# Kernel optimization log

Hardware: AMD Instinct MI355X
Metric: run time of the kernel (lower is better)

## Reference

```python
import jax, jax.numpy as jnp
import numpy as np

BOOST_STRENGTH = 1.0  # from init kwargs, already >= 0


def setup_inputs() -> dict:
    key = jax.random.key(0)
    k1, k2 = jax.random.split(key)
    B, C, H, W = 64, 128, 56, 56
    x = jax.random.normal(k1, (B, C, H, W), dtype=jnp.float32)
    # duty cycles are running activation frequencies in [0, 1]
    duty_cycles = jax.random.uniform(k2, (1, C, 1, 1), dtype=jnp.float32)
    k = 40141  # round(0.1 * C*H*W)
    return {"x": x, "duty_cycles": duty_cycles, "k": k}


def reference(x, duty_cycles, k):
    B = x.shape[0]
    n = x.shape[1] * x.shape[2] * x.shape[3]
    target_density = jnp.float32(k / n)
    # boosting only selects winners; original (unboosted) values are kept
    boost_factors = jnp.exp((target_density - duty_cycles) * BOOST_STRENGTH)
    boosted = (x * boost_factors).reshape(B, -1)   # [B, n]
    flat_x = x.reshape(B, -1)                      # [B, n]
    _, idx = jax.lax.top_k(boosted, k)             # [B, k]
    winners = jnp.take_along_axis(flat_x, idx, axis=1)  # original values at winning units
    res = jnp.zeros_like(flat_x).at[jnp.arange(B)[:, None], idx].set(winners)
    return res.reshape(x.shape)
```

## Files before the change

### kernel.cpp

```cpp
#include <hip/hip_runtime.h>
#include <stdint.h>

#define BB 64
#define CC 128
#define HW 3136
#define NPR (CC * HW)
#define NBINS 8192
#define BIN_SHIFT 19
#define KEY_LOW 0x7FFFFu

typedef float vf4 __attribute__((ext_vector_type(4)));

#define ROWMETA_OFF 512
#define COUNTER_OFF 2048
#define HIST_OFF 4096
#define CAND_OFF (HIST_OFF + (size_t)BB * NBINS * 4)

__device__ __forceinline__ uint32_t tokey(float b) {
    uint32_t u = __float_as_uint(b);
    return u ^ (uint32_t)(((int32_t)u >> 31) | 0x80000000);
}

__device__ __forceinline__ float boostf(const float* dc, int c, int K) {
    float td = (float)((double)K / (double)NPR);
    float d = td - dc[c];
    return (float)exp((double)d);
}

__global__ __launch_bounds__(256) void k_hist(const float* __restrict__ x,
                                              const float* __restrict__ dc,
                                              const int* __restrict__ kptr,
                                              uint32_t* __restrict__ hist) {
    __shared__ uint32_t lh[NBINS];
    __shared__ float sbf[8];
    for (int i = threadIdx.x; i < NBINS; i += 256) lh[i] = 0;
    if (threadIdx.x < 8) {
        int c0 = (blockIdx.x & 15) * 8;
        sbf[threadIdx.x] = boostf(dc, c0 + threadIdx.x, *kptr);
    }
    __syncthreads();

    int row = blockIdx.x >> 4;
    int c0 = (blockIdx.x & 15) * 8;
    const float4* xp = (const float4*)(x + (size_t)row * NPR + (size_t)c0 * HW);
    const int nf4 = 8 * HW / 4;

    int t = threadIdx.x;
    for (; t + 256 < nf4; t += 512) {
        float4 a = xp[t];
        float4 b = xp[t + 256];
        float fa = sbf[t / 784];
        float fb = sbf[(t + 256) / 784];
        atomicAdd(&lh[tokey(a.x * fa) >> BIN_SHIFT], 1u);
        atomicAdd(&lh[tokey(a.y * fa) >> BIN_SHIFT], 1u);
        atomicAdd(&lh[tokey(a.z * fa) >> BIN_SHIFT], 1u);
        atomicAdd(&lh[tokey(a.w * fa) >> BIN_SHIFT], 1u);
        atomicAdd(&lh[tokey(b.x * fb) >> BIN_SHIFT], 1u);
        atomicAdd(&lh[tokey(b.y * fb) >> BIN_SHIFT], 1u);
        atomicAdd(&lh[tokey(b.z * fb) >> BIN_SHIFT], 1u);
        atomicAdd(&lh[tokey(b.w * fb) >> BIN_SHIFT], 1u);
    }
    if (t < nf4) {
        float4 a = xp[t];
        float fa = sbf[t / 784];
        atomicAdd(&lh[tokey(a.x * fa) >> BIN_SHIFT], 1u);
        atomicAdd(&lh[tokey(a.y * fa) >> BIN_SHIFT], 1u);
        atomicAdd(&lh[tokey(a.z * fa) >> BIN_SHIFT], 1u);
        atomicAdd(&lh[tokey(a.w * fa) >> BIN_SHIFT], 1u);
    }
    __syncthreads();
    uint32_t* gh = hist + (size_t)row * NBINS;
    for (int i = threadIdx.x; i < NBINS; i += 256) {
        uint32_t v = lh[i];
        if (v) atomicAdd(&gh[i], v);
    }
}

__global__ __launch_bounds__(256) void k_scan(const uint32_t* __restrict__ hist,
                                              const int* __restrict__ kptr,
                                              int2* __restrict__ rowmeta) {
    int row = blockIdx.x;
    const uint32_t* gh = hist + (size_t)row * NBINS;
    uint32_t K = (uint32_t)(*kptr);
    __shared__ uint32_t csum[256];
    int t = threadIdx.x;
    int hi = NBINS - 1 - 32 * t;
    uint32_t s = 0;
    for (int j = 0; j < 32; j++) s += gh[hi - j];
    csum[t] = s;
    __syncthreads();
    for (int off = 1; off < 256; off <<= 1) {
        uint32_t v = (t >= off) ? csum[t - off] : 0u;
        __syncthreads();
        csum[t] += v;
        __syncthreads();
    }
    uint32_t incl = csum[t];
    uint32_t excl = incl - s;
    if (excl < K && incl >= K) {
        uint32_t cum = excl;
        for (int j = 0; j < 32; j++) {
            int b = hi - j;
            uint32_t h = gh[b];
            if (cum + h >= K) { rowmeta[row] = make_int2(b, (int)(K - cum)); break; }
            cum += h;
        }
    }
}

__global__ __launch_bounds__(256) void k_write(const float* __restrict__ x,
                                               const float* __restrict__ dc,
                                               const int* __restrict__ kptr,
                                               const int2* __restrict__ rowmeta,
                                               float* __restrict__ out,
                                               unsigned long long* __restrict__ cand,
                                               uint32_t* __restrict__ counters,
                                               int cap) {
    int row = blockIdx.x >> 4;
    int c0 = (blockIdx.x & 15) * 8;
    int bstar = rowmeta[row].x;

    __shared__ float sbf[8];
    __shared__ uint32_t lcnt;
    __shared__ uint32_t gbase;
    __shared__ unsigned long long lbuf[2048];
    if (threadIdx.x == 0) lcnt = 0;
    if (threadIdx.x < 8) sbf[threadIdx.x] = boostf(dc, c0 + threadIdx.x, *kptr);
    __syncthreads();

    size_t base = (size_t)row * NPR + (size_t)c0 * HW;
    const float4* xp = (const float4*)(x + base);
    vf4* op = (vf4*)(out + base);
    int jbase = c0 * HW;
    const int nf4 = 8 * HW / 4;

    int t = threadIdx.x;
    for (; t + 256 < nf4; t += 512) {
        float4 a = xp[t];
        float4 b = xp[t + 256];
        float fa = sbf[t / 784];
        float fb = sbf[(t + 256) / 784];
        vf4 oa, ob;
        float* ai = (float*)&a;
        float* bi = (float*)&b;
        #pragma unroll
        for (int q = 0; q < 4; q++) {
            float xv = ai[q];
            uint32_t key = tokey(xv * fa);
            int bin = (int)(key >> BIN_SHIFT);
            oa[q] = (bin > bstar) ? xv : 0.0f;
            if (bin == bstar) {
                uint32_t j = (uint32_t)(jbase + 4 * t + q);
                unsigned long long packed =
                    ((unsigned long long)(key & KEY_LOW) << 32) | (uint32_t)(~j);
                uint32_t pos = atomicAdd(&lcnt, 1u);
                if (pos < 2048u) lbuf[pos] = packed;
                else {
                    uint32_t gp = atomicAdd(&counters[row], 1u);
                    if ((int)gp < cap) cand[(size_t)row * cap + gp] = packed;
                }
            }
        }
        #pragma unroll
        for (int q = 0; q < 4; q++) {
            float xv = bi[q];
            uint32_t key = tokey(xv * fb);
            int bin = (int)(key >> BIN_SHIFT);
            ob[q] = (bin > bstar) ? xv : 0.0f;
            if (bin == bstar) {
                uint32_t j = (uint32_t)(jbase + 4 * (t + 256) + q);
                unsigned long long packed =
                    ((unsigned long long)(key & KEY_LOW) << 32) | (uint32_t)(~j);
                uint32_t pos = atomicAdd(&lcnt, 1u);
                if (pos < 2048u) lbuf[pos] = packed;
                else {
                    uint32_t gp = atomicAdd(&counters[row], 1u);
                    if ((int)gp < cap) cand[(size_t)row * cap + gp] = packed;
                }
            }
        }
        __builtin_nontemporal_store(oa, &op[t]);
        __builtin_nontemporal_store(ob, &op[t + 256]);
    }
    if (t < nf4) {
        float4 a = xp[t];
        float fa = sbf[t / 784];
        vf4 oa;
        float* ai = (float*)&a;
        #pragma unroll
        for (int q = 0; q < 4; q++) {
            float xv = ai[q];
            uint32_t key = tokey(xv * fa);
            int bin = (int)(key >> BIN_SHIFT);
            oa[q] = (bin > bstar) ? xv : 0.0f;
            if (bin == bstar) {
                uint32_t j = (uint32_t)(jbase + 4 * t + q);
                unsigned long long packed =
                    ((unsigned long long)(key & KEY_LOW) << 32) | (uint32_t)(~j);
                uint32_t pos = atomicAdd(&lcnt, 1u);
                if (pos < 2048u) lbuf[pos] = packed;
                else {
                    uint32_t gp = atomicAdd(&counters[row], 1u);
                    if ((int)gp < cap) cand[(size_t)row * cap + gp] = packed;
                }
            }
        }
        __builtin_nontemporal_store(oa, &op[t]);
    }
    __syncthreads();
    uint32_t m = lcnt < 2048u ? lcnt : 2048u;
    if (threadIdx.x == 0) gbase = atomicAdd(&counters[row], m);
    __syncthreads();
    for (uint32_t i = threadIdx.x; i < m; i += 256) {
        uint32_t pos = gbase + i;
        if ((int)pos < cap) cand[(size_t)row * cap + pos] = lbuf[i];
    }
}

__global__ __launch_bounds__(1024) void k_select(const float* __restrict__ x,
                                                 float* __restrict__ out,
                                                 const unsigned long long* __restrict__ cand,
                                                 const uint32_t* __restrict__ counters,
                                                 const int2* __restrict__ rowmeta,
                                                 int cap) {
    int row = blockIdx.x;
    uint32_t cnt = counters[row];
    if ((int)cnt > cap) cnt = (uint32_t)cap;
    int E = rowmeta[row].y;
    const unsigned long long* cp = cand + (size_t)row * cap;
    int tid = threadIdx.x;

    __shared__ uint32_t hist[256];
    __shared__ uint32_t sufs[256];
    __shared__ unsigned long long buf[6144];
    __shared__ uint32_t scnt;
    __shared__ int sh_d, sh_done;

    unsigned long long prefix = 0ull, mask = 0ull, thr = 0ull;
    uint32_t remaining = (uint32_t)E;
    bool compacted = false;
    uint32_t csize = cnt;
    if (tid == 0) sh_done = 0;

    for (int shift = 48; shift >= 0; shift -= 8) {
        if (tid < 256) hist[tid] = 0;
        __syncthreads();
        if (!compacted) {
            for (uint32_t s = tid; s < cnt; s += 1024) {
                unsigned long long v = cp[s];
                if ((v & mask) == prefix)
                    atomicAdd(&hist[(uint32_t)(v >> shift) & 255u], 1u);
            }
        } else {
            for (uint32_t s = tid; s < csize; s += 1024)
                atomicAdd(&hist[(uint32_t)(buf[s] >> shift) & 255u], 1u);
        }
        __syncthreads();
        if (tid < 256) sufs[tid] = hist[tid];
        __syncthreads();
        for (int off = 1; off < 256; off <<= 1) {
            uint32_t add = 0;
            if (tid < 256 && tid + off < 256) add = sufs[tid + off];
            __syncthreads();
            if (tid < 256) sufs[tid] += add;
            __syncthreads();
        }
        if (tid < 256) {
            uint32_t sd = sufs[tid];
            uint32_t sn = (tid < 255) ? sufs[tid + 1] : 0u;
            if (sd >= remaining && sn < remaining) sh_d = tid;
        }
        __syncthreads();
        int d = sh_d;
        uint32_t cumG = (d < 255) ? sufs[d + 1] : 0u;
        uint32_t binC = sufs[d] - cumG;
        unsigned long long npref = prefix | ((unsigned long long)(uint32_t)d << shift);
        bool done = (sufs[d] == remaining);
        if (done) {
            thr = npref;
            if (tid == 0) sh_done = 1;
        }
        remaining -= cumG;
        __syncthreads();
        if (!sh_done && binC <= 6144u && shift > 0) {
            if (tid == 0) scnt = 0;
            unsigned long long keep[6]; int nk = 0;
            if (compacted) {
                for (uint32_t s = tid; s < csize; s += 1024) {
                    unsigned long long v = buf[s];
                    if (((uint32_t)(v >> shift) & 255u) == (uint32_t)d) {
                        if (nk < 6) keep[nk++] = v;
                    }
                }
            }
            __syncthreads();
            if (!compacted) {
                for (uint32_t s = tid; s < cnt; s += 1024) {
                    unsigned long long v = cp[s];
                    if ((v & mask) == prefix &&
                        ((uint32_t)(v >> shift) & 255u) == (uint32_t)d) {
                        uint32_t p = atomicAdd(&scnt, 1u);
                        buf[p] = v;
                    }
                }
            } else if (nk > 0) {
                uint32_t p = atomicAdd(&scnt, (uint32_t)nk);
                for (int i = 0; i < nk; i++) buf[p + i] = keep[i];
            }
            __syncthreads();
            csize = binC;
            compacted = true;
        }
        prefix = npref;
        mask |= (0xFFull << shift);
        if (sh_done) break;
    }
    if (!sh_done) thr = prefix;

    const float* xr = x + (size_t)row * NPR;
    float* orow = out + (size_t)row * NPR;
    for (uint32_t s = tid; s < cnt; s += 1024) {
        unsigned long long v = cp[s];
        if (v >= thr) {
            uint32_t j = ~(uint32_t)v;
            orow[j] = xr[j];
        }
    }
}

extern "C" void kernel_launch(void* const* d_in, const int* in_sizes, int n_in,
                              void* d_out, int out_size, void* d_ws, size_t ws_size,
                              hipStream_t stream) {
    const float* x  = (const float*)d_in[0];
    const float* dc = (const float*)d_in[1];
    const int* kptr = (const int*)d_in[2];
    float* out = (float*)d_out;

    char* ws = (char*)d_ws;
    int2* rowmeta       = (int2*)(ws + ROWMETA_OFF);
    uint32_t* counters  = (uint32_t*)(ws + COUNTER_OFF);
    uint32_t* hist      = (uint32_t*)(ws + HIST_OFF);
    unsigned long long* cand = (unsigned long long*)(ws + CAND_OFF);

    size_t cap_sz = (ws_size > CAND_OFF) ? (ws_size - CAND_OFF) / ((size_t)BB * 8) : 0;
    if (cap_sz > 65536) cap_sz = 65536;
    int cap = (int)cap_sz;

    (void)hipMemsetAsync(ws, 0, CAND_OFF, stream);
    k_hist<<<BB * 16, 256, 0, stream>>>(x, dc, kptr, hist);
    k_scan<<<BB, 256, 0, stream>>>(hist, kptr, rowmeta);
    k_write<<<BB * 16, 256, 0, stream>>>(x, dc, kptr, rowmeta, out, cand, counters, cap);
    k_select<<<BB, 1024, 0, stream>>>(x, out, cand, counters, rowmeta, cap);
}
```

Measured before the change: 224.2 us.

## Fuse row scan and select into last-arriving block via done counters

Removes the separate k_scan and k_select launches. The last of the 16 blocks per row now does the threshold scan at the end of k_hist and the radix select at the end of k_write, detected through atomic done counters. Select runs with 256 threads and reuses the 2048-entry lbuf shared buffer instead of a 6144-entry buffer, so the compaction threshold is lower. This saves launch gaps and tail latency, but the per-row select runs on fewer threads and is serialized behind the slowest block of each row.

```diff
diff --git a/kernel.cpp b/kernel.cpp
--- a/kernel.cpp
+++ b/kernel.cpp
@@ -13,6 +13,8 @@
 
 #define ROWMETA_OFF 512
 #define COUNTER_OFF 2048
+#define DONE1_OFF 2560
+#define DONE2_OFF 2816
 #define HIST_OFF 4096
 #define CAND_OFF (HIST_OFF + (size_t)BB * NBINS * 4)
 
@@ -27,12 +29,23 @@
     return (float)exp((double)d);
 }
 
+__device__ __forceinline__ uint32_t aload32(const uint32_t* p) {
+    return __hip_atomic_load(p, __ATOMIC_RELAXED, __HIP_MEMORY_SCOPE_AGENT);
+}
+__device__ __forceinline__ unsigned long long aload64(const unsigned long long* p) {
+    return __hip_atomic_load(p, __ATOMIC_RELAXED, __HIP_MEMORY_SCOPE_AGENT);
+}
+
 __global__ __launch_bounds__(256) void k_hist(const float* __restrict__ x,
                                               const float* __restrict__ dc,
                                               const int* __restrict__ kptr,
-                                              uint32_t* __restrict__ hist) {
+                                              uint32_t* __restrict__ hist,
+                                              uint32_t* __restrict__ done1,
+                                              int2* __restrict__ rowmeta) {
     __shared__ uint32_t lh[NBINS];
     __shared__ float sbf[8];
+    __shared__ uint32_t csum[256];
+    __shared__ int sh_last;
     for (int i = threadIdx.x; i < NBINS; i += 256) lh[i] = 0;
     if (threadIdx.x < 8) {
         int c0 = (blockIdx.x & 15) * 8;
@@ -74,34 +87,35 @@
         uint32_t v = lh[i];
         if (v) atomicAdd(&gh[i], v);
     }
-}
-
-__global__ __launch_bounds__(256) void k_scan(const uint32_t* __restrict__ hist,
-                                              const int* __restrict__ kptr,
-                                              int2* __restrict__ rowmeta) {
-    int row = blockIdx.x;
-    const uint32_t* gh = hist + (size_t)row * NBINS;
+
+    if (threadIdx.x == 0) {
+        uint32_t prev = __hip_atomic_fetch_add(&done1[row], 1u,
+                          __ATOMIC_ACQ_REL, __HIP_MEMORY_SCOPE_AGENT);
+        sh_last = (prev == 15);
+    }
+    __syncthreads();
+    if (!sh_last) return;
+
     uint32_t K = (uint32_t)(*kptr);
-    __shared__ uint32_t csum[256];
-    int t = threadIdx.x;
-    int hi = NBINS - 1 - 32 * t;
+    int tt = threadIdx.x;
+    int hi = NBINS - 1 - 32 * tt;
     uint32_t s = 0;
-    for (int j = 0; j < 32; j++) s += gh[hi - j];
-    csum[t] = s;
+    for (int j = 0; j < 32; j++) s += aload32(&gh[hi - j]);
+    csum[tt] = s;
     __syncthreads();
     for (int off = 1; off < 256; off <<= 1) {
-        uint32_t v = (t >= off) ? csum[t - off] : 0u;
-        __syncthreads();
-        csum[t] += v;
-        __syncthreads();
-    }
-    uint32_t incl = csum[t];
+        uint32_t v = (tt >= off) ? csum[tt - off] : 0u;
+        __syncthreads();
+        csum[tt] += v;
+        __syncthreads();
+    }
+    uint32_t incl = csum[tt];
     uint32_t excl = incl - s;
     if (excl < K && incl >= K) {
         uint32_t cum = excl;
         for (int j = 0; j < 32; j++) {
             int b = hi - j;
-            uint32_t h = gh[b];
+            uint32_t h = aload32(&gh[b]);
             if (cum + h >= K) { rowmeta[row] = make_int2(b, (int)(K - cum)); break; }
             cum += h;
         }
@@ -115,15 +129,17 @@
                                                float* __restrict__ out,
                                                unsigned long long* __restrict__ cand,
                                                uint32_t* __restrict__ counters,
+                                               uint32_t* __restrict__ done2,
                                                int cap) {
     int row = blockIdx.x >> 4;
     int c0 = (blockIdx.x & 15) * 8;
-    int bstar = rowmeta[row].x;
+    int2 rm = rowmeta[row];
+    int bstar = rm.x;
 
     __shared__ float sbf[8];
-    __shared__ uint32_t lcnt;
-    __shared__ uint32_t gbase;
+    __shared__ uint32_t lcnt, gbase;
     __shared__ unsigned long long lbuf[2048];
+    __shared__ int sh_last;
     if (threadIdx.x == 0) lcnt = 0;
     if (threadIdx.x < 8) sbf[threadIdx.x] = boostf(dc, c0 + threadIdx.x, *kptr);
     __syncthreads();
@@ -215,57 +231,54 @@
         uint32_t pos = gbase + i;
         if ((int)pos < cap) cand[(size_t)row * cap + pos] = lbuf[i];
     }
-}
-
-__global__ __launch_bounds__(1024) void k_select(const float* __restrict__ x,
-                                                 float* __restrict__ out,
-                                                 const unsigned long long* __restrict__ cand,
-                                                 const uint32_t* __restrict__ counters,
-                                                 const int2* __restrict__ rowmeta,
-                                                 int cap) {
-    int row = blockIdx.x;
-    uint32_t cnt = counters[row];
+
+    if (threadIdx.x == 0) {
+        uint32_t prev = __hip_atomic_fetch_add(&done2[row], 1u,
+                          __ATOMIC_ACQ_REL, __HIP_MEMORY_SCOPE_AGENT);
+        sh_last = (prev == 15);
+    }
+    __syncthreads();
+    if (!sh_last) return;
+
+    uint32_t cnt = aload32(&counters[row]);
     if ((int)cnt > cap) cnt = (uint32_t)cap;
-    int E = rowmeta[row].y;
+    uint32_t remaining = (uint32_t)rm.y;
     const unsigned long long* cp = cand + (size_t)row * cap;
     int tid = threadIdx.x;
 
-    __shared__ uint32_t hist[256];
+    __shared__ uint32_t hh[256];
     __shared__ uint32_t sufs[256];
-    __shared__ unsigned long long buf[6144];
     __shared__ uint32_t scnt;
     __shared__ int sh_d, sh_done;
 
     unsigned long long prefix = 0ull, mask = 0ull, thr = 0ull;
-    uint32_t remaining = (uint32_t)E;
     bool compacted = false;
     uint32_t csize = cnt;
     if (tid == 0) sh_done = 0;
 
     for (int shift = 48; shift >= 0; shift -= 8) {
-        if (tid < 256) hist[tid] = 0;
+        hh[tid] = 0;
         __syncthreads();
         if (!compacted) {
-            for (uint32_t s = tid; s < cnt; s += 1024) {
-                unsigned long long v = cp[s];
+            for (uint32_t s = tid; s < cnt; s += 256) {
+                unsigned long long v = aload64(&cp[s]);
                 if ((v & mask) == prefix)
-                    atomicAdd(&hist[(uint32_t)(v >> shift) & 255u], 1u);
+                    atomicAdd(&hh[(uint32_t)(v >> shift) & 255u], 1u);
             }
         } else {
-            for (uint32_t s = tid; s < csize; s += 1024)
-                atomicAdd(&hist[(uint32_t)(buf[s] >> shift) & 255u], 1u);
-        }
-        __syncthreads();
-        if (tid < 256) sufs[tid] = hist[tid];
+            for (uint32_t s = tid; s < csize; s += 256)
+                atomicAdd(&hh[(uint32_t)(lbuf[s] >> shift) & 255u], 1u);
+        }
+        __syncthreads();
+        sufs[tid] = hh[tid];
         __syncthreads();
         for (int off = 1; off < 256; off <<= 1) {
-            uint32_t add = 0;
-            if (tid < 256 && tid + off < 256) add = sufs[tid + off];
+            uint32_t add = (tid + off < 256) ? sufs[tid + off] : 0u;
             __syncthreads();
-            if (tid < 256) sufs[tid] += add;
+            sufs[tid] += add;
             __syncthreads();
         }
-        if (tid < 256) {
+        {
             uint32_t sd = sufs[tid];
             uint32_t sn = (tid < 255) ? sufs[tid + 1] : 0u;
             if (sd >= remaining && sn < remaining) sh_d = tid;
@@ -275,37 +288,36 @@
         uint32_t cumG = (d < 255) ? sufs[d + 1] : 0u;
         uint32_t binC = sufs[d] - cumG;
         unsigned long long npref = prefix | ((unsigned long long)(uint32_t)d << shift);
-        bool done = (sufs[d] == remaining);
-        if (done) {
+        bool done_ = (sufs[d] == remaining);
+        if (done_) {
             thr = npref;
             if (tid == 0) sh_done = 1;
         }
         remaining -= cumG;
         __syncthreads();
-        if (!sh_done && binC <= 6144u && shift > 0) {
+        if (!sh_done && binC <= 2048u && shift > 0) {
             if (tid == 0) scnt = 0;
-            unsigned long long keep[6]; int nk = 0;
+            unsigned long long keep[8]; int nk = 0;
             if (compacted) {
-                for (uint32_t s = tid; s < csize; s += 1024) {
-                    unsigned long long v = buf[s];
-                    if (((uint32_t)(v >> shift) & 255u) == (uint32_t)d) {
-                        if (nk < 6) keep[nk++] = v;
-                    }
+                for (uint32_t s = tid; s < csize; s += 256) {
+                    unsigned long long v = lbuf[s];
+                    if (((uint32_t)(v >> shift) & 255u) == (uint32_t)d && nk < 8)
+                        keep[nk++] = v;
                 }
             }
             __syncthreads();
             if (!compacted) {
-                for (uint32_t s = tid; s < cnt; s += 1024) {
-                    unsigned long long v = cp[s];
+                for (uint32_t s = tid; s < cnt; s += 256) {
+                    unsigned long long v = aload64(&cp[s]);
                     if ((v & mask) == prefix &&
                         ((uint32_t)(v >> shift) & 255u) == (uint32_t)d) {
                         uint32_t p = atomicAdd(&scnt, 1u);
-                        buf[p] = v;
+                        lbuf[p] = v;
                     }
                 }
             } else if (nk > 0) {
                 uint32_t p = atomicAdd(&scnt, (uint32_t)nk);
-                for (int i = 0; i < nk; i++) buf[p + i] = keep[i];
+                for (int i = 0; i < nk; i++) lbuf[p + i] = keep[i];
             }
             __syncthreads();
             csize = binC;
@@ -319,8 +331,8 @@
 
     const float* xr = x + (size_t)row * NPR;
     float* orow = out + (size_t)row * NPR;
-    for (uint32_t s = tid; s < cnt; s += 1024) {
-        unsigned long long v = cp[s];
+    for (uint32_t s = tid; s < cnt; s += 256) {
+        unsigned long long v = aload64(&cp[s]);
         if (v >= thr) {
             uint32_t j = ~(uint32_t)v;
             orow[j] = xr[j];
@@ -339,6 +351,8 @@
     char* ws = (char*)d_ws;
     int2* rowmeta       = (int2*)(ws + ROWMETA_OFF);
     uint32_t* counters  = (uint32_t*)(ws + COUNTER_OFF);
+    uint32_t* done1     = (uint32_t*)(ws + DONE1_OFF);
+    uint32_t* done2     = (uint32_t*)(ws + DONE2_OFF);
     uint32_t* hist      = (uint32_t*)(ws + HIST_OFF);
     unsigned long long* cand = (unsigned long long*)(ws + CAND_OFF);
 
@@ -347,8 +361,6 @@
     int cap = (int)cap_sz;
 
     (void)hipMemsetAsync(ws, 0, CAND_OFF, stream);
-    k_hist<<<BB * 16, 256, 0, stream>>>(x, dc, kptr, hist);
-    k_scan<<<BB, 256, 0, stream>>>(hist, kptr, rowmeta);
-    k_write<<<BB * 16, 256, 0, stream>>>(x, dc, kptr, rowmeta, out, cand, counters, cap);
-    k_select<<<BB, 1024, 0, stream>>>(x, out, cand, counters, rowmeta, cap);
-}
+    k_hist<<<BB * 16, 256, 0, stream>>>(x, dc, kptr, hist, done1, rowmeta);
+    k_write<<<BB * 16, 256, 0, stream>>>(x, dc, kptr, rowmeta, out, cand, counters, done2, cap);
+}
```

After: 292.8 us. 1.31x slower.

## Replace full histogram pass with sampled threshold bracketing for top-k selection

Applied to the files above, without the earlier changes.

Drops the full-tensor histogram pass and the scan kernel. A new sampling kernel estimates upper and lower key thresholds per row from about 8K strided samples with a margin. The streaming pass then writes certain winners directly and pushes in-between candidates with wave-aggregated atomics. A final kernel radix-selects among the candidates, and if the bracket was wrong it falls back to a per-row full histogram path. This removes one full read of the input in the common case, but a bad sample triggers a slow single-block-per-row fallback.

```diff
diff --git a/kernel.cpp b/kernel.cpp
--- a/kernel.cpp
+++ b/kernel.cpp
@@ -5,16 +5,19 @@
 #define CC 128
 #define HW 3136
 #define NPR (CC * HW)
-#define NBINS 8192
-#define BIN_SHIFT 19
-#define KEY_LOW 0x7FFFFu
+#define NF4 (NPR / 4)
+#define F4CH (HW / 4)
+#define SS 2048
+#define SSTRIDE 49
+#define MARGIN 400
 
 typedef float vf4 __attribute__((ext_vector_type(4)));
 
-#define ROWMETA_OFF 512
-#define COUNTER_OFF 2048
-#define HIST_OFF 4096
-#define CAND_OFF (HIST_OFF + (size_t)BB * NBINS * 4)
+#define THI_OFF 0
+#define TLO_OFF 256
+#define CHI_OFF 512
+#define CNT_OFF 768
+#define CAND_OFF 4096
 
 __device__ __forceinline__ uint32_t tokey(float b) {
     uint32_t u = __float_as_uint(b);
@@ -27,103 +30,197 @@
     return (float)exp((double)d);
 }
 
-__global__ __launch_bounds__(256) void k_hist(const float* __restrict__ x,
-                                              const float* __restrict__ dc,
-                                              const int* __restrict__ kptr,
-                                              uint32_t* __restrict__ hist) {
-    __shared__ uint32_t lh[NBINS];
-    __shared__ float sbf[8];
-    for (int i = threadIdx.x; i < NBINS; i += 256) lh[i] = 0;
-    if (threadIdx.x < 8) {
-        int c0 = (blockIdx.x & 15) * 8;
-        sbf[threadIdx.x] = boostf(dc, c0 + threadIdx.x, *kptr);
-    }
-    __syncthreads();
-
+__device__ uint32_t select32(const uint32_t* kreg, uint32_t m,
+                             uint32_t* hh, uint32_t* sufs, int* sh_d) {
+    int tid = threadIdx.x;
+    uint32_t prefix = 0, mask = 0, remaining = m;
+    for (int shift = 24; shift >= 0; shift -= 8) {
+        if (tid < 256) hh[tid] = 0;
+        __syncthreads();
+        #pragma unroll
+        for (int i = 0; i < 8; i++) {
+            uint32_t v = kreg[i];
+            if ((v & mask) == prefix) atomicAdd(&hh[(v >> shift) & 255u], 1u);
+        }
+        __syncthreads();
+        if (tid < 256) sufs[tid] = hh[tid];
+        __syncthreads();
+        for (int off = 1; off < 256; off <<= 1) {
+            uint32_t add = 0;
+            if (tid < 256 && tid + off < 256) add = sufs[tid + off];
+            __syncthreads();
+            if (tid < 256) sufs[tid] += add;
+            __syncthreads();
+        }
+        if (tid < 256) {
+            uint32_t sd = sufs[tid], sn = (tid < 255) ? sufs[tid + 1] : 0u;
+            if (sd >= remaining && sn < remaining) *sh_d = tid;
+        }
+        __syncthreads();
+        int d = *sh_d;
+        uint32_t cumG = (d < 255) ? sufs[d + 1] : 0u;
+        prefix |= ((uint32_t)d << shift);
+        mask |= (0xFFu << shift);
+        remaining -= cumG;
+        __syncthreads();
+    }
+    return prefix;
+}
+
+__device__ unsigned long long select64(const unsigned long long* cp, uint32_t cnt,
+                                       uint32_t E, uint32_t* hh, uint32_t* sufs,
+                                       unsigned long long* lbuf, uint32_t* scnt,
+                                       int* sh_d, int* sh_done) {
+    int tid = threadIdx.x, nt = blockDim.x;
+    unsigned long long prefix = 0ull, mask = 0ull, thr = 0ull;
+    uint32_t remaining = E, csize = cnt;
+    bool compacted = false;
+    if (tid == 0) *sh_done = 0;
+    __syncthreads();
+    for (int shift = 56; shift >= 0; shift -= 8) {
+        if (tid < 256) hh[tid] = 0;
+        __syncthreads();
+        if (!compacted) {
+            for (uint32_t s = tid; s < cnt; s += nt) {
+                unsigned long long v = cp[s];
+                if ((v & mask) == prefix)
+                    atomicAdd(&hh[(uint32_t)(v >> shift) & 255u], 1u);
+            }
+        } else {
+            for (uint32_t s = tid; s < csize; s += nt)
+                atomicAdd(&hh[(uint32_t)(lbuf[s] >> shift) & 255u], 1u);
+        }
+        __syncthreads();
+        if (tid < 256) sufs[tid] = hh[tid];
+        __syncthreads();
+        for (int off = 1; off < 256; off <<= 1) {
+            uint32_t add = 0;
+            if (tid < 256 && tid + off < 256) add = sufs[tid + off];
+            __syncthreads();
+            if (tid < 256) sufs[tid] += add;
+            __syncthreads();
+        }
+        if (tid < 256) {
+            uint32_t sd = sufs[tid], sn = (tid < 255) ? sufs[tid + 1] : 0u;
+            if (sd >= remaining && sn < remaining) *sh_d = tid;
+        }
+        __syncthreads();
+        int d = *sh_d;
+        uint32_t cumG = (d < 255) ? sufs[d + 1] : 0u;
+        uint32_t binC = sufs[d] - cumG;
+        unsigned long long npref = prefix | ((unsigned long long)(uint32_t)d << shift);
+        bool done_ = (sufs[d] == remaining);
+        if (done_) { thr = npref; if (tid == 0) *sh_done = 1; }
+        remaining -= cumG;
+        __syncthreads();
+        if (!*sh_done && binC <= 4096u && shift > 0) {
+            if (tid == 0) *scnt = 0;
+            unsigned long long keep[8]; int nk = 0;
+            if (compacted) {
+                for (uint32_t s = tid; s < csize; s += nt) {
+                    unsigned long long v = lbuf[s];
+                    if (((uint32_t)(v >> shift) & 255u) == (uint32_t)d && nk < 8)
+                        keep[nk++] = v;
+                }
+            }
+            __syncthreads();
+            if (!compacted) {
+                for (uint32_t s = tid; s < cnt; s += nt) {
+                    unsigned long long v = cp[s];
+                    if ((v & mask) == prefix &&
+                        ((uint32_t)(v >> shift) & 255u) == (uint32_t)d)
+                        lbuf[atomicAdd(scnt, 1u)] = v;
+                }
+            } else if (nk > 0) {
+                uint32_t p = atomicAdd(scnt, (uint32_t)nk);
+                for (int i = 0; i < nk; i++) lbuf[p + i] = keep[i];
+            }
+            __syncthreads();
+            csize = binC;
+            compacted = true;
+        }
+        prefix = npref;
+        mask |= (0xFFull << shift);
+        if (*sh_done) break;
+    }
+    __syncthreads();
+    if (!*sh_done) thr = prefix;
+    return thr;
+}
+
+__global__ __launch_bounds__(1024) void k_sample(const float* __restrict__ x,
+                                                 const float* __restrict__ dc,
+                                                 const int* __restrict__ kptr,
+                                                 uint32_t* __restrict__ thi,
+                                                 uint32_t* __restrict__ tlo) {
+    __shared__ float sbf[CC];
+    __shared__ uint32_t hh[256], sufs[256];
+    __shared__ int sh_d;
+    int row = blockIdx.x, tid = threadIdx.x;
+    int K = *kptr;
+    if (tid < CC) sbf[tid] = boostf(dc, tid, K);
+    __syncthreads();
+    const float4* xp = (const float4*)(x + (size_t)row * NPR);
+    uint32_t kreg[8];
+    #pragma unroll
+    for (int h = 0; h < 2; h++) {
+        int u = tid + h * 1024;
+        float4 v = xp[(size_t)u * SSTRIDE];
+        float f = sbf[u >> 4];
+        kreg[4*h+0] = tokey(v.x * f); kreg[4*h+1] = tokey(v.y * f);
+        kreg[4*h+2] = tokey(v.z * f); kreg[4*h+3] = tokey(v.w * f);
+    }
+    int S = SS * 4;
+    int m_mid = (int)(((long long)K * S) / NPR);
+    int m_hi = m_mid - MARGIN; if (m_hi < 1) m_hi = 1;
+    int m_lo = m_mid + MARGIN; if (m_lo > S) m_lo = S;
+    uint32_t t1 = select32(kreg, (uint32_t)m_hi, hh, sufs, &sh_d);
+    __syncthreads();
+    uint32_t t2 = select32(kreg, (uint32_t)m_lo, hh, sufs, &sh_d);
+    if (tid == 0) { thi[row] = t1; tlo[row] = t2; }
+}
+
+__device__ __forceinline__ void push_cand(bool isc, unsigned long long packed,
+                                          uint32_t* lcnt, unsigned long long* lbuf,
+                                          uint32_t* counters, unsigned long long* cand,
+                                          int row, int cap) {
+    unsigned long long ball = __ballot(isc);
+    uint32_t tot = (uint32_t)__popcll(ball);
+    if (tot == 0) return;
+    uint32_t lo = (uint32_t)ball, hi = (uint32_t)(ball >> 32);
+    uint32_t lanepre = __builtin_amdgcn_mbcnt_hi(hi, __builtin_amdgcn_mbcnt_lo(lo, 0));
+    int leader = __ffsll((unsigned long long)ball) - 1;
+    uint32_t base = 0;
+    if (isc && lanepre == 0) base = atomicAdd(lcnt, tot);
+    base = __shfl(base, leader, 64);
+    if (isc) {
+        uint32_t pos = base + lanepre;
+        if (pos < 4096u) lbuf[pos] = packed;
+        else {
+            uint32_t gp = atomicAdd(&counters[row], 1u);
+            if ((int)gp < cap) cand[(size_t)row * cap + gp] = packed;
+        }
+    }
+}
+
+__global__ __launch_bounds__(256) void k_stream(const float* __restrict__ x,
+                                                const float* __restrict__ dc,
+                                                const int* __restrict__ kptr,
+                                                const uint32_t* __restrict__ thi,
+                                                const uint32_t* __restrict__ tlo,
+                                                float* __restrict__ out,
+                                                unsigned long long* __restrict__ cand,
+                                                uint32_t* __restrict__ counters,
+                                                uint32_t* __restrict__ chi,
+                                                int cap) {
     int row = blockIdx.x >> 4;
     int c0 = (blockIdx.x & 15) * 8;
-    const float4* xp = (const float4*)(x + (size_t)row * NPR + (size_t)c0 * HW);
-    const int nf4 = 8 * HW / 4;
-
-    int t = threadIdx.x;
-    for (; t + 256 < nf4; t += 512) {
-        float4 a = xp[t];
-        float4 b = xp[t + 256];
-        float fa = sbf[t / 784];
-        float fb = sbf[(t + 256) / 784];
-        atomicAdd(&lh[tokey(a.x * fa) >> BIN_SHIFT], 1u);
-        atomicAdd(&lh[tokey(a.y * fa) >> BIN_SHIFT], 1u);
-        atomicAdd(&lh[tokey(a.z * fa) >> BIN_SHIFT], 1u);
-        atomicAdd(&lh[tokey(a.w * fa) >> BIN_SHIFT], 1u);
-        atomicAdd(&lh[tokey(b.x * fb) >> BIN_SHIFT], 1u);
-        atomicAdd(&lh[tokey(b.y * fb) >> BIN_SHIFT], 1u);
-        atomicAdd(&lh[tokey(b.z * fb) >> BIN_SHIFT], 1u);
-        atomicAdd(&lh[tokey(b.w * fb) >> BIN_SHIFT], 1u);
-    }
-    if (t < nf4) {
-        float4 a = xp[t];
-        float fa = sbf[t / 784];
-        atomicAdd(&lh[tokey(a.x * fa) >> BIN_SHIFT], 1u);
-        atomicAdd(&lh[tokey(a.y * fa) >> BIN_SHIFT], 1u);
-        atomicAdd(&lh[tokey(a.z * fa) >> BIN_SHIFT], 1u);
-        atomicAdd(&lh[tokey(a.w * fa) >> BIN_SHIFT], 1u);
-    }
-    __syncthreads();
-    uint32_t* gh = hist + (size_t)row * NBINS;
-    for (int i = threadIdx.x; i < NBINS; i += 256) {
-        uint32_t v = lh[i];
-        if (v) atomicAdd(&gh[i], v);
-    }
-}
-
-__global__ __launch_bounds__(256) void k_scan(const uint32_t* __restrict__ hist,
-                                              const int* __restrict__ kptr,
-                                              int2* __restrict__ rowmeta) {
-    int row = blockIdx.x;
-    const uint32_t* gh = hist + (size_t)row * NBINS;
-    uint32_t K = (uint32_t)(*kptr);
-    __shared__ uint32_t csum[256];
-    int t = threadIdx.x;
-    int hi = NBINS - 1 - 32 * t;
-    uint32_t s = 0;
-    for (int j = 0; j < 32; j++) s += gh[hi - j];
-    csum[t] = s;
-    __syncthreads();
-    for (int off = 1; off < 256; off <<= 1) {
-        uint32_t v = (t >= off) ? csum[t - off] : 0u;
-        __syncthreads();
-        csum[t] += v;
-        __syncthreads();
-    }
-    uint32_t incl = csum[t];
-    uint32_t excl = incl - s;
-    if (excl < K && incl >= K) {
-        uint32_t cum = excl;
-        for (int j = 0; j < 32; j++) {
-            int b = hi - j;
-            uint32_t h = gh[b];
-            if (cum + h >= K) { rowmeta[row] = make_int2(b, (int)(K - cum)); break; }
-            cum += h;
-        }
-    }
-}
-
-__global__ __launch_bounds__(256) void k_write(const float* __restrict__ x,
-                                               const float* __restrict__ dc,
-                                               const int* __restrict__ kptr,
-                                               const int2* __restrict__ rowmeta,
-                                               float* __restrict__ out,
-                                               unsigned long long* __restrict__ cand,
-                                               uint32_t* __restrict__ counters,
-                                               int cap) {
-    int row = blockIdx.x >> 4;
-    int c0 = (blockIdx.x & 15) * 8;
-    int bstar = rowmeta[row].x;
+    uint32_t Thi = thi[row], Tlo = tlo[row];
 
     __shared__ float sbf[8];
-    __shared__ uint32_t lcnt;
-    __shared__ uint32_t gbase;
-    __shared__ unsigned long long lbuf[2048];
+    __shared__ uint32_t lcnt, gbase;
+    __shared__ unsigned long long lbuf[4096];
+    __shared__ uint32_t red[256];
     if (threadIdx.x == 0) lcnt = 0;
     if (threadIdx.x < 8) sbf[threadIdx.x] = boostf(dc, c0 + threadIdx.x, *kptr);
     __syncthreads();
@@ -133,13 +230,14 @@
     vf4* op = (vf4*)(out + base);
     int jbase = c0 * HW;
     const int nf4 = 8 * HW / 4;
+    uint32_t myhi = 0;
 
     int t = threadIdx.x;
     for (; t + 256 < nf4; t += 512) {
         float4 a = xp[t];
         float4 b = xp[t + 256];
-        float fa = sbf[t / 784];
-        float fb = sbf[(t + 256) / 784];
+        float fa = sbf[t / F4CH];
+        float fb = sbf[(t + 256) / F4CH];
         vf4 oa, ob;
         float* ai = (float*)&a;
         float* bi = (float*)&b;
@@ -147,184 +245,168 @@
         for (int q = 0; q < 4; q++) {
             float xv = ai[q];
             uint32_t key = tokey(xv * fa);
-            int bin = (int)(key >> BIN_SHIFT);
-            oa[q] = (bin > bstar) ? xv : 0.0f;
-            if (bin == bstar) {
-                uint32_t j = (uint32_t)(jbase + 4 * t + q);
-                unsigned long long packed =
-                    ((unsigned long long)(key & KEY_LOW) << 32) | (uint32_t)(~j);
-                uint32_t pos = atomicAdd(&lcnt, 1u);
-                if (pos < 2048u) lbuf[pos] = packed;
-                else {
-                    uint32_t gp = atomicAdd(&counters[row], 1u);
-                    if ((int)gp < cap) cand[(size_t)row * cap + gp] = packed;
-                }
-            }
+            bool win = key > Thi;
+            myhi += win;
+            oa[q] = win ? xv : 0.0f;
+            bool isc = (!win) && (key > Tlo);
+            uint32_t j = (uint32_t)(jbase + 4 * t + q);
+            unsigned long long packed = ((unsigned long long)key << 32) | (uint32_t)(~j);
+            push_cand(isc, packed, &lcnt, lbuf, counters, cand, row, cap);
         }
         #pragma unroll
         for (int q = 0; q < 4; q++) {
             float xv = bi[q];
             uint32_t key = tokey(xv * fb);
-            int bin = (int)(key >> BIN_SHIFT);
-            ob[q] = (bin > bstar) ? xv : 0.0f;
-            if (bin == bstar) {
-                uint32_t j = (uint32_t)(jbase + 4 * (t + 256) + q);
-                unsigned long long packed =
-                    ((unsigned long long)(key & KEY_LOW) << 32) | (uint32_t)(~j);
-                uint32_t pos = atomicAdd(&lcnt, 1u);
-                if (pos < 2048u) lbuf[pos] = packed;
-                else {
-                    uint32_t gp = atomicAdd(&counters[row], 1u);
-                    if ((int)gp < cap) cand[(size_t)row * cap + gp] = packed;
-                }
-            }
+            bool win = key > Thi;
+            myhi += win;
+            ob[q] = win ? xv : 0.0f;
+            bool isc = (!win) && (key > Tlo);
+            uint32_t j = (uint32_t)(jbase + 4 * (t + 256) + q);
+            unsigned long long packed = ((unsigned long long)key << 32) | (uint32_t)(~j);
+            push_cand(isc, packed, &lcnt, lbuf, counters, cand, row, cap);
         }
         __builtin_nontemporal_store(oa, &op[t]);
         __builtin_nontemporal_store(ob, &op[t + 256]);
     }
     if (t < nf4) {
         float4 a = xp[t];
-        float fa = sbf[t / 784];
+        float fa = sbf[t / F4CH];
         vf4 oa;
         float* ai = (float*)&a;
         #pragma unroll
         for (int q = 0; q < 4; q++) {
             float xv = ai[q];
             uint32_t key = tokey(xv * fa);
-            int bin = (int)(key >> BIN_SHIFT);
-            oa[q] = (bin > bstar) ? xv : 0.0f;
-            if (bin == bstar) {
-                uint32_t j = (uint32_t)(jbase + 4 * t + q);
-                unsigned long long packed =
-                    ((unsigned long long)(key & KEY_LOW) << 32) | (uint32_t)(~j);
-                uint32_t pos = atomicAdd(&lcnt, 1u);
-                if (pos < 2048u) lbuf[pos] = packed;
-                else {
-                    uint32_t gp = atomicAdd(&counters[row], 1u);
-                    if ((int)gp < cap) cand[(size_t)row * cap + gp] = packed;
-                }
-            }
+            bool win = key > Thi;
+            myhi += win;
+            oa[q] = win ? xv : 0.0f;
+            bool isc = (!win) && (key > Tlo);
+            uint32_t j = (uint32_t)(jbase + 4 * t + q);
+            unsigned long long packed = ((unsigned long long)key << 32) | (uint32_t)(~j);
+            push_cand(isc, packed, &lcnt, lbuf, counters, cand, row, cap);
         }
         __builtin_nontemporal_store(oa, &op[t]);
     }
     __syncthreads();
-    uint32_t m = lcnt < 2048u ? lcnt : 2048u;
+    uint32_t m = lcnt < 4096u ? lcnt : 4096u;
     if (threadIdx.x == 0) gbase = atomicAdd(&counters[row], m);
     __syncthreads();
     for (uint32_t i = threadIdx.x; i < m; i += 256) {
         uint32_t pos = gbase + i;
         if ((int)pos < cap) cand[(size_t)row * cap + pos] = lbuf[i];
     }
-}
-
-__global__ __launch_bounds__(1024) void k_select(const float* __restrict__ x,
-                                                 float* __restrict__ out,
-                                                 const unsigned long long* __restrict__ cand,
-                                                 const uint32_t* __restrict__ counters,
-                                                 const int2* __restrict__ rowmeta,
-                                                 int cap) {
-    int row = blockIdx.x;
-    uint32_t cnt = counters[row];
-    if ((int)cnt > cap) cnt = (uint32_t)cap;
-    int E = rowmeta[row].y;
-    const unsigned long long* cp = cand + (size_t)row * cap;
-    int tid = threadIdx.x;
-
-    __shared__ uint32_t hist[256];
-    __shared__ uint32_t sufs[256];
-    __shared__ unsigned long long buf[6144];
+    red[threadIdx.x] = myhi;
+    __syncthreads();
+    for (int off = 128; off > 0; off >>= 1) {
+        if ((int)threadIdx.x < off) red[threadIdx.x] += red[threadIdx.x + off];
+        __syncthreads();
+    }
+    if (threadIdx.x == 0) atomicAdd(&chi[row], red[0]);
+}
+
+__global__ __launch_bounds__(1024) void k_final(const float* __restrict__ x,
+                                                const float* __restrict__ dc,
+                                                const int* __restrict__ kptr,
+                                                float* __restrict__ out,
+                                                unsigned long long* __restrict__ cand,
+                                                const uint32_t* __restrict__ counters,
+                                                const uint32_t* __restrict__ chi,
+                                                int cap) {
+    __shared__ uint32_t hh[256], sufs[256];
+    __shared__ unsigned long long lbuf[4096];
+    __shared__ uint32_t cs1024[1024];
+    __shared__ float sbf[CC];
     __shared__ uint32_t scnt;
-    __shared__ int sh_d, sh_done;
-
-    unsigned long long prefix = 0ull, mask = 0ull, thr = 0ull;
-    uint32_t remaining = (uint32_t)E;
-    bool compacted = false;
-    uint32_t csize = cnt;
-    if (tid == 0) sh_done = 0;
-
-    for (int shift = 48; shift >= 0; shift -= 8) {
-        if (tid < 256) hist[tid] = 0;
-        __syncthreads();
-        if (!compacted) {
-            for (uint32_t s = tid; s < cnt; s += 1024) {
-                unsigned long long v = cp[s];
-                if ((v & mask) == prefix)
-                    atomicAdd(&hist[(uint32_t)(v >> shift) & 255u], 1u);
-            }
-        } else {
-            for (uint32_t s = tid; s < csize; s += 1024)
-                atomicAdd(&hist[(uint32_t)(buf[s] >> shift) & 255u], 1u);
-        }
-        __syncthreads();
-        if (tid < 256) sufs[tid] = hist[tid];
-        __syncthreads();
-        for (int off = 1; off < 256; off <<= 1) {
-            uint32_t add = 0;
-            if (tid < 256 && tid + off < 256) add = sufs[tid + off];
-            __syncthreads();
-            if (tid < 256) sufs[tid] += add;
-            __syncthreads();
-        }
-        if (tid < 256) {
-            uint32_t sd = sufs[tid];
-            uint32_t sn = (tid < 255) ? sufs[tid + 1] : 0u;
-            if (sd >= remaining && sn < remaining) sh_d = tid;
-        }
-        __syncthreads();
-        int d = sh_d;
-        uint32_t cumG = (d < 255) ? sufs[d + 1] : 0u;
-        uint32_t binC = sufs[d] - cumG;
-        unsigned long long npref = prefix | ((unsigned long long)(uint32_t)d << shift);
-        bool done = (sufs[d] == remaining);
-        if (done) {
-            thr = npref;
-            if (tid == 0) sh_done = 1;
-        }
-        remaining -= cumG;
-        __syncthreads();
-        if (!sh_done && binC <= 6144u && shift > 0) {
-            if (tid == 0) scnt = 0;
-            unsigned long long keep[6]; int nk = 0;
-            if (compacted) {
-                for (uint32_t s = tid; s < csize; s += 1024) {
-                    unsigned long long v = buf[s];
-                    if (((uint32_t)(v >> shift) & 255u) == (uint32_t)d) {
-                        if (nk < 6) keep[nk++] = v;
-                    }
-                }
-            }
-            __syncthreads();
-            if (!compacted) {
-                for (uint32_t s = tid; s < cnt; s += 1024) {
-                    unsigned long long v = cp[s];
-                    if ((v & mask) == prefix &&
-                        ((uint32_t)(v >> shift) & 255u) == (uint32_t)d) {
-                        uint32_t p = atomicAdd(&scnt, 1u);
-                        buf[p] = v;
-                    }
-                }
-            } else if (nk > 0) {
-                uint32_t p = atomicAdd(&scnt, (uint32_t)nk);
-                for (int i = 0; i < nk; i++) buf[p + i] = keep[i];
-            }
-            __syncthreads();
-            csize = binC;
-            compacted = true;
-        }
-        prefix = npref;
-        mask |= (0xFFull << shift);
-        if (sh_done) break;
-    }
-    if (!sh_done) thr = prefix;
-
+    __shared__ int sh_d, sh_done, sh_b, sh_E;
+    int row = blockIdx.x, tid = threadIdx.x;
+    int K = *kptr;
+    uint32_t cnt = counters[row], c_hi = chi[row];
+    long long E = (long long)K - (long long)c_hi;
+    unsigned long long* cp = cand + (size_t)row * cap;
     const float* xr = x + (size_t)row * NPR;
     float* orow = out + (size_t)row * NPR;
-    for (uint32_t s = tid; s < cnt; s += 1024) {
+
+    bool ok = (E >= 0) && (E <= (long long)cnt) && ((int)cnt <= cap);
+    if (ok) {
+        if (E == 0) return;
+        unsigned long long thr = select64(cp, cnt, (uint32_t)E, hh, sufs,
+                                          lbuf, &scnt, &sh_d, &sh_done);
+        for (uint32_t s = tid; s < cnt; s += 1024) {
+            unsigned long long v = cp[s];
+            if (v >= thr) { uint32_t j = ~(uint32_t)v; orow[j] = xr[j]; }
+        }
+        return;
+    }
+
+    uint32_t* lh = (uint32_t*)lbuf;
+    if (tid < CC) sbf[tid] = boostf(dc, tid, K);
+    for (int i = tid; i < 8192; i += 1024) lh[i] = 0;
+    __syncthreads();
+    const float4* xp = (const float4*)xr;
+    for (int t = tid; t < NF4; t += 1024) {
+        float4 v = xp[t];
+        float f = sbf[t / F4CH];
+        atomicAdd(&lh[tokey(v.x * f) >> 19], 1u);
+        atomicAdd(&lh[tokey(v.y * f) >> 19], 1u);
+        atomicAdd(&lh[tokey(v.z * f) >> 19], 1u);
+        atomicAdd(&lh[tokey(v.w * f) >> 19], 1u);
+    }
+    __syncthreads();
+    {
+        int hi = 8191 - 8 * tid;
+        uint32_t s = 0;
+        for (int j = 0; j < 8; j++) s += lh[hi - j];
+        cs1024[tid] = s;
+        __syncthreads();
+        for (int off = 1; off < 1024; off <<= 1) {
+            uint32_t v = (tid >= off) ? cs1024[tid - off] : 0u;
+            __syncthreads();
+            cs1024[tid] += v;
+            __syncthreads();
+        }
+        uint32_t incl = cs1024[tid], excl = incl - s;
+        if (excl < (uint32_t)K && incl >= (uint32_t)K) {
+            uint32_t cum = excl;
+            for (int j = 0; j < 8; j++) {
+                int b = hi - j;
+                uint32_t h = lh[b];
+                if (cum + h >= (uint32_t)K) { sh_b = b; sh_E = (int)((uint32_t)K - cum); break; }
+                cum += h;
+            }
+        }
+    }
+    __syncthreads();
+    int bstar = sh_b;
+    uint32_t E2 = (uint32_t)sh_E;
+    if (tid == 0) scnt = 0;
+    __syncthreads();
+    for (int t = tid; t < NF4; t += 1024) {
+        float4 v = xp[t];
+        float f = sbf[t / F4CH];
+        vf4 o;
+        float* vi = (float*)&v;
+        #pragma unroll
+        for (int q = 0; q < 4; q++) {
+            float xv = vi[q];
+            uint32_t key = tokey(xv * f);
+            int bin = (int)(key >> 19);
+            o[q] = (bin > bstar) ? xv : 0.0f;
+            if (bin == bstar) {
+                uint32_t j = (uint32_t)(4 * t + q);
+                unsigned long long packed = ((unsigned long long)key << 32) | (uint32_t)(~j);
+                uint32_t p = atomicAdd(&scnt, 1u);
+                if ((int)p < cap) cp[p] = packed;
+            }
+        }
+        ((vf4*)orow)[t] = o;
+    }
+    __syncthreads();
+    uint32_t cnt2 = scnt;
+    if ((int)cnt2 > cap) cnt2 = (uint32_t)cap;
+    unsigned long long thr = select64(cp, cnt2, E2, hh, sufs, lbuf, &scnt, &sh_d, &sh_done);
+    for (uint32_t s = tid; s < cnt2; s += 1024) {
         unsigned long long v = cp[s];
-        if (v >= thr) {
-            uint32_t j = ~(uint32_t)v;
-            orow[j] = xr[j];
-        }
+        if (v >= thr) { uint32_t j = ~(uint32_t)v; orow[j] = xr[j]; }
     }
 }
 
@@ -337,18 +419,18 @@
     float* out = (float*)d_out;
 
     char* ws = (char*)d_ws;
-    int2* rowmeta       = (int2*)(ws + ROWMETA_OFF);
-    uint32_t* counters  = (uint32_t*)(ws + COUNTER_OFF);
-    uint32_t* hist      = (uint32_t*)(ws + HIST_OFF);
+    uint32_t* thi      = (uint32_t*)(ws + THI_OFF);
+    uint32_t* tlo      = (uint32_t*)(ws + TLO_OFF);
+    uint32_t* chi      = (uint32_t*)(ws + CHI_OFF);
+    uint32_t* counters = (uint32_t*)(ws + CNT_OFF);
     unsigned long long* cand = (unsigned long long*)(ws + CAND_OFF);
 
     size_t cap_sz = (ws_size > CAND_OFF) ? (ws_size - CAND_OFF) / ((size_t)BB * 8) : 0;
     if (cap_sz > 65536) cap_sz = 65536;
     int cap = (int)cap_sz;
 
-    (void)hipMemsetAsync(ws, 0, CAND_OFF, stream);
-    k_hist<<<BB * 16, 256, 0, stream>>>(x, dc, kptr, hist);
-    k_scan<<<BB, 256, 0, stream>>>(hist, kptr, rowmeta);
-    k_write<<<BB * 16, 256, 0, stream>>>(x, dc, kptr, rowmeta, out, cand, counters, cap);
-    k_select<<<BB, 1024, 0, stream>>>(x, out, cand, counters, rowmeta, cap);
-}
+    (void)hipMemsetAsync(ws, 0, 4096, stream);
+    k_sample<<<BB, 1024, 0, stream>>>(x, dc, kptr, thi, tlo);
+    k_stream<<<BB * 16, 256, 0, stream>>>(x, dc, kptr, thi, tlo, out, cand, counters, chi, cap);
+    k_final<<<BB, 1024, 0, stream>>>(x, dc, kptr, out, cand, counters, chi, cap);
+}
```

Result: slower. 346.7 us (+54.7%).
